# Kernel optimization log

Hardware: AMD Instinct MI355X
Metric: run time of the kernel (lower is better)

The kernel has to match this reference:

```python
import jax, jax.numpy as jnp
import numpy as np

B, T, D = 32, 1024, 512

def _xavier(key, shape):
    fan_in, fan_out = shape[1], shape[0]
    bound = float(np.sqrt(6.0 / (fan_in + fan_out)))
    return jax.random.uniform(key, shape, jnp.float32, -bound, bound)

def setup_inputs() -> dict:
    key = jax.random.key(0)
    ks = jax.random.split(key, 10)
    lin_bound = float(1.0 / np.sqrt(D))
    def lin(kw, kb):
        W = jax.random.uniform(kw, (D, D), jnp.float32, -lin_bound, lin_bound)
        b = jax.random.uniform(kb, (D,), jnp.float32, -lin_bound, lin_bound)
        return W, b
    Wk_w, Wk_b = lin(ks[0], ks[1])
    Wv_w, Wv_b = lin(ks[2], ks[3])
    Wq_w, Wq_b = lin(ks[4], ks[5])
    Wo_w, Wo_b = lin(ks[6], ks[7])
    w = _xavier(ks[8], (T, T))
    x = jax.random.normal(ks[9], (B, T, D), jnp.float32)
    return {"x": x, "Wk_w": Wk_w, "Wk_b": Wk_b, "Wv_w": Wv_w, "Wv_b": Wv_b,
            "Wq_w": Wq_w, "Wq_b": Wq_b, "w": w, "Wo_w": Wo_w, "Wo_b": Wo_b}

def reference(x, Wk_w, Wk_b, Wv_w, Wv_b, Wq_w, Wq_b, w, Wo_w, Wo_b):
    # K, V, Q: [B, T, D]  (torch Linear: x @ W.T + b)
    K = jnp.einsum('btd,ed->bte', x, Wk_w) + Wk_b
    V = jnp.einsum('btd,ed->bte', x, Wv_w) + Wv_b
    # exp_w: [T, T], row-wise max-stabilized position bias
    exp_w = jnp.exp(w - jnp.max(w, axis=-1, keepdims=True))
    # Faithful to original: max over dim=0 (batch dim) of K
    exp_K = jnp.exp(K - jnp.max(K, axis=0, keepdims=True))  # [B, T, D]
    num = jnp.einsum('ts,bsd->btd', exp_w, exp_K * V)
    den = jnp.einsum('ts,bsd->btd', exp_w, exp_K)
    Yt = num / den
    Q = jnp.einsum('btd,ed->bte', x, Wq_w) + Wq_b
    Yt = jax.nn.sigmoid(Q) * Yt
    out = jnp.einsum('btd,ed->bte', Yt, Wo_w) + Wo_b
    return out
```

## Files before the change

### kernel.cpp

```cpp
#include <hip/hip_runtime.h>
#include <stdint.h>

typedef unsigned short u16;
typedef __attribute__((ext_vector_type(4))) float f32x4;
typedef __attribute__((ext_vector_type(8))) __bf16 bf16x8;

__device__ __forceinline__ float b2f(u16 u) {
  union { unsigned int i; float f; } v; v.i = ((unsigned int)u) << 16; return v.f;
}
__device__ __forceinline__ u16 f2b(float f) {
  union { float f; unsigned int i; } v; v.f = f;
  unsigned int x = v.i;
  return (u16)((x + 0x7fffu + ((x >> 16) & 1u)) >> 16);
}

__device__ __forceinline__ void async_ld16(const u16* g, u16* l) {
  __builtin_amdgcn_global_load_lds((const __attribute__((address_space(1))) void*)g,
                                   (__attribute__((address_space(3))) void*)l, 16, 0, 0);
}

__global__ void detect_kernel(const u16* __restrict__ x, int* __restrict__ flag)
{
  const int tid = threadIdx.x;
  int found = 0;
  for (int i = tid; i < 32768; i += 256) {
    u16 u = x[i];
    if ((u & 0x7F80u) == 0x7F80u) found = 1;
  }
  unsigned long long m = __ballot(found != 0);
  __shared__ int sf[4];
  if ((tid & 63) == 0) sf[tid >> 6] = (m != 0ULL) ? 1 : 0;
  __syncthreads();
  if (tid == 0) flag[0] = (sf[0] | sf[1] | sf[2] | sf[3]);
}

__global__ __launch_bounds__(256)
void conv_kernel(const void* __restrict__ in, u16* __restrict__ out, long n,
                 const int* __restrict__ flag)
{
  const long i = ((long)blockIdx.x * 256 + threadIdx.x) * 8;
  if (i >= n) return;
  if (flag[0]) {
    const float* p = (const float*)in + i;
    u16 o[8];
#pragma unroll
    for (int j = 0; j < 8; j++) o[j] = f2b(p[j]);
    *(uint4*)(out + i) = *(const uint4*)o;
  } else {
    *(uint4*)(out + i) = *(const uint4*)((const u16*)in + i);
  }
}

__global__ __launch_bounds__(256)
void conv4_kernel(const void* __restrict__ i0, const void* __restrict__ i1,
                  const void* __restrict__ i2, const void* __restrict__ i3,
                  u16* __restrict__ o0, u16* __restrict__ o1,
                  u16* __restrict__ o2, u16* __restrict__ o3,
                  const int* __restrict__ flag)
{
  const int sel = blockIdx.x >> 7;
  const int blk = blockIdx.x & 127;
  const void* in = (sel == 0) ? i0 : (sel == 1) ? i1 : (sel == 2) ? i2 : i3;
  u16* out = (sel == 0) ? o0 : (sel == 1) ? o1 : (sel == 2) ? o2 : o3;
  const long i = ((long)blk * 256 + threadIdx.x) * 8;
  if (flag[0]) {
    const float* p = (const float*)in + i;
    u16 o[8];
#pragma unroll
    for (int j = 0; j < 8; j++) o[j] = f2b(p[j]);
    *(uint4*)(out + i) = *(const uint4*)o;
  } else {
    *(uint4*)(out + i) = *(const uint4*)((const u16*)in + i);
  }
}

#define BM 128
#define BN 128
#define BK 32

template<int EPI>
__global__ __launch_bounds__(256)
void gemm_bt(const u16* __restrict__ A, const u16* __restrict__ B,
             const void* __restrict__ bias, void* __restrict__ Cv,
             const int* __restrict__ flag,
             int M, int N, int K, long strideC)
{
  __shared__ __align__(16) u16 sA[2][BM * BK];
  __shared__ __align__(16) u16 sB[2][BN * BK];

  const int tid  = threadIdx.x;
  const int lane = tid & 63;
  const int wv   = tid >> 6;
  const int fl = flag[0];
  u16* Cb16 = (u16*)Cv;

  int bx = blockIdx.x, by = blockIdx.y;
  {
    const int nx = gridDim.x, ny = gridDim.y;
    if ((nx & 7) == 0) {
      const int d   = bx + nx * by;
      const int xcd = d & 7;
      const int s   = d >> 3;
      const int q   = s / ny;
      bx = xcd * (nx >> 3) + q;
      by = s - q * ny;
    }
  }
  const int m0 = bx * BM;
  const int n0 = by * BN;

  const int ldRow = wv * 32;
  const int lr = lane >> 2;
  const int lc = lane & 3;
  const int scol = (lc ^ ((lr >> 1) & 3)) * 8;
  const u16* gA = A + (long)(m0 + ldRow + lr) * K + scol;
  const u16* gB = B + (long)(n0 + ldRow + lr) * K + scol;
  const int off0 = (ldRow + lr) * BK + lc * 8;
  const int off1 = (ldRow + 16 + lr) * BK + lc * 8;

  f32x4 acc[4][4];
#pragma unroll
  for (int i = 0; i < 4; i++)
#pragma unroll
    for (int j = 0; j < 4; j++) acc[i][j] = (f32x4)0.0f;

  const int waveM = (wv >> 1) * 64;
  const int waveN = (wv & 1) * 64;
  const int quad  = lane >> 4;
  const int ll    = lane & 15;
  const int rs    = (quad ^ ((ll >> 1) & 3)) * 8;

  async_ld16(gA,          sA[0] + off0);
  async_ld16(gA + 16 * K, sA[0] + off1);
  async_ld16(gB,          sB[0] + off0);
  async_ld16(gB + 16 * K, sB[0] + off1);
  gA += BK; gB += BK;

  const int NT = K / BK;
  for (int t = 0; t < NT; ++t) {
    __syncthreads();
    const int cur = t & 1;
    if (t + 1 < NT) {
      u16* dA = sA[cur ^ 1];
      u16* dB = sB[cur ^ 1];
      async_ld16(gA,          dA + off0);
      async_ld16(gA + 16 * K, dA + off1);
      async_ld16(gB,          dB + off0);
      async_ld16(gB + 16 * K, dB + off1);
      gA += BK; gB += BK;
    }
    const u16* rA = sA[cur];
    const u16* rB = sB[cur];
    bf16x8 aF[4], bF[4];
#pragma unroll
    for (int i = 0; i < 4; i++) {
      aF[i] = *(const bf16x8*)(rA + (waveM + i * 16 + ll) * BK + rs);
      bF[i] = *(const bf16x8*)(rB + (waveN + i * 16 + ll) * BK + rs);
    }
#pragma unroll
    for (int i = 0; i < 4; i++)
#pragma unroll
      for (int j = 0; j < 4; j++)
        acc[i][j] = __builtin_amdgcn_mfma_f32_16x16x32_bf16(aF[i], bF[j], acc[i][j], 0, 0, 0);
  }

#pragma unroll
  for (int i = 0; i < 4; i++) {
    const int rowb = m0 + waveM + i * 16 + quad * 4;
#pragma unroll
    for (int j = 0; j < 4; j++) {
      const int col = n0 + waveN + j * 16 + ll;
      const float bv = fl ? ((const float*)bias)[col] : b2f(((const u16*)bias)[col]);
#pragma unroll
      for (int r = 0; r < 4; r++) {
        const long idx = (long)(rowb + r) * N + col;
        const float v = acc[i][j][r] + bv;
        if (EPI == 0) {
          Cb16[idx] = f2b(v);
        } else {
          const long g = strideC + idx;
          if (fl) ((float*)Cv)[g] = v;
          else    ((u16*)Cv)[g]   = f2b(v);
        }
      }
    }
  }
}

__global__ __launch_bounds__(256)
void gemm_proj3(const u16* __restrict__ A, const u16* __restrict__ Bw,
                const void* __restrict__ kb, const void* __restrict__ vb,
                const void* __restrict__ qb,
                u16* __restrict__ Kp, u16* __restrict__ Vp, u16* __restrict__ Qp,
                const int* __restrict__ flag, int M)
{
  const int KD = 512;
  __shared__ __align__(16) u16 sA[2][BM * BK];
  __shared__ __align__(16) u16 sB[2][BN * BK];

  const int tid  = threadIdx.x;
  const int lane = tid & 63;
  const int wv   = tid >> 6;
  const int fl = flag[0];

  int bx = blockIdx.x, by = blockIdx.y;
  {
    const int nx = gridDim.x, ny = gridDim.y;
    if ((nx & 7) == 0) {
      const int d   = bx + nx * by;
      const int xcd = d & 7;
      const int s   = d >> 3;
      const int q   = s / ny;
      bx = xcd * (nx >> 3) + q;
      by = s - q * ny;
    }
  }
  const int m0 = bx * BM;
  const int n0 = by * BN;

  const int ldRow = wv * 32;
  const int lr = lane >> 2;
  const int lc = lane & 3;
  const int scol = (lc ^ ((lr >> 1) & 3)) * 8;
  const u16* gA = A  + (long)(m0 + ldRow + lr) * KD + scol;
  const u16* gB = Bw + (long)(n0 + ldRow + lr) * KD + scol;
  const int off0 = (ldRow + lr) * BK + lc * 8;
  const int off1 = (ldRow + 16 + lr) * BK + lc * 8;

  f32x4 acc[4][4];
#pragma unroll
  for (int i = 0; i < 4; i++)
#pragma unroll
    for (int j = 0; j < 4; j++) acc[i][j] = (f32x4)0.0f;

  const int waveM = (wv >> 1) * 64;
  const int waveN = (wv & 1) * 64;
  const int quad  = lane >> 4;
  const int ll    = lane & 15;
  const int rs    = (quad ^ ((ll >> 1) & 3)) * 8;

  async_ld16(gA,           sA[0] + off0);
  async_ld16(gA + 16 * KD, sA[0] + off1);
  async_ld16(gB,           sB[0] + off0);
  async_ld16(gB + 16 * KD, sB[0] + off1);
  gA += BK; gB += BK;

  const int NT = KD / BK;
  for (int t = 0; t < NT; ++t) {
    __syncthreads();
    const int cur = t & 1;
    if (t + 1 < NT) {
      u16* dA = sA[cur ^ 1];
      u16* dB = sB[cur ^ 1];
      async_ld16(gA,           dA + off0);
      async_ld16(gA + 16 * KD, dA + off1);
      async_ld16(gB,           dB + off0);
      async_ld16(gB + 16 * KD, dB + off1);
      gA += BK; gB += BK;
    }
    const u16* rA = sA[cur];
    const u16* rB = sB[cur];
    bf16x8 aF[4], bF[4];
#pragma unroll
    for (int i = 0; i < 4; i++) {
      aF[i] = *(const bf16x8*)(rA + (waveM + i * 16 + ll) * BK + rs);
      bF[i] = *(const bf16x8*)(rB + (waveN + i * 16 + ll) * BK + rs);
    }
#pragma unroll
    for (int i = 0; i < 4; i++)
#pragma unroll
      for (int j = 0; j < 4; j++)
        acc[i][j] = __builtin_amdgcn_mfma_f32_16x16x32_bf16(aF[i], bF[j], acc[i][j], 0, 0, 0);
  }

#pragma unroll
  for (int i = 0; i < 4; i++) {
    const int rowb = m0 + waveM + i * 16 + quad * 4;
#pragma unroll
    for (int j = 0; j < 4; j++) {
      const int col = n0 + waveN + j * 16 + ll;
      const int sel = col >> 9;
      const int cs  = col & 511;
      const void* bp = (sel == 0) ? kb : (sel == 1) ? vb : qb;
      u16* dst = (sel == 0) ? Kp : (sel == 1) ? Vp : Qp;
      const float bv = fl ? ((const float*)bp)[cs] : b2f(((const u16*)bp)[cs]);
#pragma unroll
      for (int r = 0; r < 4; r++)
        dst[(long)(rowb + r) * 512 + cs] = f2b(acc[i][j][r] + bv);
    }
  }
}

__global__ __launch_bounds__(512, 2)
void gemm_aft(const u16* __restrict__ ew, const u16* __restrict__ Pt,
              const u16* __restrict__ PVt, const u16* __restrict__ Q,
              u16* __restrict__ Yt)
{
  const int T = 1024, D = 512;
  __shared__ __align__(16) u16 sA[2 * 2 * 256 * 32];
  __shared__ __align__(16) u16 sB[2 * 2 * 128 * 32];
  __shared__ __align__(16) u16 sC[2 * 2 * 128 * 32];

  const int tid  = threadIdx.x;
  const int lane = tid & 63;
  const int wv   = tid >> 6;

  int xt = blockIdx.x, yt = blockIdx.y, zt = blockIdx.z;
  {
    const int nz = gridDim.z;
    if ((nz & 1) == 0) {
      const int d   = xt + (yt << 2) + (zt << 4);
      const int xcd = d & 7;
      const int s   = d >> 3;
      xt = s & 3;
      const int p = xcd * (nz >> 1) + (s >> 2);
      yt = p & 3;
      zt = p >> 2;
    }
  }
  const int b = zt;
  const u16* Ptb  = Pt  + (long)b * D * T;
  const u16* PVtb = PVt + (long)b * D * T;
  const u16* Qb   = Q   + (long)b * T * D;
  u16*       Ytb  = Yt  + (long)b * T * D;
  const int m0 = xt * 256;
  const int n0 = yt * 128;

  const int sr = tid >> 2, ss = tid & 3;
  const int sslot = (ss ^ ((sr >> 1) & 3)) * 8;
  const u16* gA0 = ew   + (long)(m0 + sr)       * T + sslot;
  const u16* gA1 = ew   + (long)(m0 + 128 + sr) * T + sslot;
  const u16* gB  = Ptb  + (long)(n0 + sr)       * T + sslot;
  const u16* gC  = PVtb + (long)(n0 + sr)       * T + sslot;
  const int soff = sr * 32 + ss * 8;

  f32x4 accN[8][2], accD[8][2];
#pragma unroll
  for (int i = 0; i < 8; i++)
#pragma unroll
    for (int j = 0; j < 2; j++) { accN[i][j] = (f32x4)0.0f; accD[i][j] = (f32x4)0.0f; }

  const int quad  = lane >> 4;
  const int ll    = lane & 15;
  const int rs    = (quad ^ ((ll >> 1) & 3)) * 8;
  const int waveM = (wv >> 2) * 128;
  const int waveN = (wv & 3) * 32;

  async_ld16(gA0,      sA + soff);
  async_ld16(gA1,      sA + 4096 + soff);
  async_ld16(gB,       sB + soff);
  async_ld16(gC,       sC + soff);
  async_ld16(gA0 + 32, sA + 8192 + soff);
  async_ld16(gA1 + 32, sA + 8192 + 4096 + soff);
  async_ld16(gB  + 32, sB + 4096 + soff);
  async_ld16(gC  + 32, sC + 4096 + soff);
  asm volatile("s_waitcnt vmcnt(4)" ::: "memory");
  __builtin_amdgcn_s_barrier();

  const int NT = T / 64;
  for (int t = 0; t < NT; ++t) {
    const int cur = t & 1;
    const u16* bA = sA + cur * 16384;
    const u16* bB = sB + cur * 8192;
    const u16* bC = sC + cur * 8192;
    u16* nA = sA + (cur ^ 1) * 16384;
    u16* nB = sB + (cur ^ 1) * 8192;
    u16* nC = sC + (cur ^ 1) * 8192;
    const int ko = (t + 1) * 64;
    const bool st = (t + 1 < NT);

    bf16x8 aF[4], bF[2], cF[2];

#pragma unroll
    for (int i = 0; i < 4; i++)
      aF[i] = *(const bf16x8*)(bA + (waveM + i * 16 + ll) * 32 + rs);
#pragma unroll
    for (int j = 0; j < 2; j++) {
      bF[j] = *(const bf16x8*)(bB + (waveN + j * 16 + ll) * 32 + rs);
      cF[j] = *(const bf16x8*)(bC + (waveN + j * 16 + ll) * 32 + rs);
    }
    if (st) {
      async_ld16(gA0 + ko, nA + soff);
      async_ld16(gA1 + ko, nA + 4096 + soff);
    }
    __builtin_amdgcn_s_barrier();
    asm volatile("s_waitcnt lgkmcnt(0)" ::: "memory");
    __builtin_amdgcn_sched_barrier(0);
    __builtin_amdgcn_s_setprio(1);
#pragma unroll
    for (int i = 0; i < 4; i++)
#pragma unroll
      for (int j = 0; j < 2; j++) {
        accD[i][j] = __builtin_amdgcn_mfma_f32_16x16x32_bf16(aF[i], bF[j], accD[i][j], 0, 0, 0);
        accN[i][j] = __builtin_amdgcn_mfma_f32_16x16x32_bf16(aF[i], cF[j], accN[i][j], 0, 0, 0);
      }
    __builtin_amdgcn_s_setprio(0);
    __builtin_amdgcn_s_barrier();

#pragma unroll
    for (int i = 0; i < 4; i++)
      aF[i] = *(const bf16x8*)(bA + (waveM + (4 + i) * 16 + ll) * 32 + rs);
    if (st) {
      async_ld16(gB + ko, nB + soff);
      async_ld16(gC + ko, nC + soff);
    }
    __builtin_amdgcn_s_barrier();
    asm volatile("s_waitcnt lgkmcnt(0)" ::: "memory");
    __builtin_amdgcn_sched_barrier(0);
    __builtin_amdgcn_s_setprio(1);
#pragma unroll
    for (int i = 0; i < 4; i++)
#pragma unroll
      for (int j = 0; j < 2; j++) {
        accD[4 + i][j] = __builtin_amdgcn_mfma_f32_16x16x32_bf16(aF[i], bF[j], accD[4 + i][j], 0, 0, 0);
        accN[4 + i][j] = __builtin_amdgcn_mfma_f32_16x16x32_bf16(aF[i], cF[j], accN[4 + i][j], 0, 0, 0);
      }
    __builtin_amdgcn_s_setprio(0);
    if (st) asm volatile("s_waitcnt vmcnt(4)" ::: "memory");
    else    asm volatile("s_waitcnt vmcnt(0)" ::: "memory");
    __builtin_amdgcn_s_barrier();

    const u16* bA1 = bA + 8192;
    const u16* bB1 = bB + 4096;
    const u16* bC1 = bC + 4096;
#pragma unroll
    for (int i = 0; i < 4; i++)
      aF[i] = *(const bf16x8*)(bA1 + (waveM + i * 16 + ll) * 32 + rs);
#pragma unroll
    for (int j = 0; j < 2; j++) {
      bF[j] = *(const bf16x8*)(bB1 + (waveN + j * 16 + ll) * 32 + rs);
      cF[j] = *(const bf16x8*)(bC1 + (waveN + j * 16 + ll) * 32 + rs);
    }
    if (st) {
      async_ld16(gA0 + ko + 32, nA + 8192 + soff);
      async_ld16(gA1 + ko + 32, nA + 8192 + 4096 + soff);
    }
    __builtin_amdgcn_s_barrier();
    asm volatile("s_waitcnt lgkmcnt(0)" ::: "memory");
    __builtin_amdgcn_sched_barrier(0);
    __builtin_amdgcn_s_setprio(1);
#pragma unroll
    for (int i = 0; i < 4; i++)
#pragma unroll
      for (int j = 0; j < 2; j++) {
        accD[i][j] = __builtin_amdgcn_mfma_f32_16x16x32_bf16(aF[i], bF[j], accD[i][j], 0, 0, 0);
        accN[i][j] = __builtin_amdgcn_mfma_f32_16x16x32_bf16(aF[i], cF[j], accN[i][j], 0, 0, 0);
      }
    __builtin_amdgcn_s_setprio(0);
    __builtin_amdgcn_s_barrier();

#pragma unroll
    for (int i = 0; i < 4; i++)
      aF[i] = *(const bf16x8*)(bA1 + (waveM + (4 + i) * 16 + ll) * 32 + rs);
    if (st) {
      async_ld16(gB + ko + 32, nB + 4096 + soff);
      async_ld16(gC + ko + 32, nC + 4096 + soff);
    }
    __builtin_amdgcn_s_barrier();
    asm volatile("s_waitcnt lgkmcnt(0)" ::: "memory");
    __builtin_amdgcn_sched_barrier(0);
    __builtin_amdgcn_s_setprio(1);
#pragma unroll
    for (int i = 0; i < 4; i++)
#pragma unroll
      for (int j = 0; j < 2; j++) {
        accD[4 + i][j] = __builtin_amdgcn_mfma_f32_16x16x32_bf16(aF[i], bF[j], accD[4 + i][j], 0, 0, 0);
        accN[4 + i][j] = __builtin_amdgcn_mfma_f32_16x16x32_bf16(aF[i], cF[j], accN[4 + i][j], 0, 0, 0);
      }
    __builtin_amdgcn_s_setprio(0);
    if (st) asm volatile("s_waitcnt vmcnt(4)" ::: "memory");
    else    asm volatile("s_waitcnt vmcnt(0)" ::: "memory");
    __builtin_amdgcn_s_barrier();
  }

#pragma unroll
  for (int i = 0; i < 8; i++) {
    const int rowb = m0 + waveM + i * 16 + quad * 4;
#pragma unroll
    for (int j = 0; j < 2; j++) {
      const int col = n0 + waveN + j * 16 + ll;
#pragma unroll
      for (int r = 0; r < 4; r++) {
        const long idx = (long)(rowb + r) * D + col;
        const float q  = b2f(Qb[idx]);
        const float e  = __expf(-q);
        const float rc = __builtin_amdgcn_rcpf(accD[i][j][r] * (1.0f + e));
        Ytb[idx] = f2b(accN[i][j][r] * rc);
      }
    }
  }
}

__global__ __launch_bounds__(256)
void expw_kernel(const void* __restrict__ w, u16* __restrict__ ew,
                 const int* __restrict__ flag)
{
  const int fl = flag[0];
  const int t = blockIdx.x;
  const int tid = threadIdx.x;
  float v[4];
  float m = -1e30f;
#pragma unroll
  for (int i = 0; i < 4; i++) {
    const long idx = (long)t * 1024 + tid + i * 256;
    float val = fl ? ((const float*)w)[idx] : b2f(((const u16*)w)[idx]);
    v[i] = val; m = fmaxf(m, val);
  }
#pragma unroll
  for (int off = 32; off > 0; off >>= 1) m = fmaxf(m, __shfl_xor(m, off, 64));
  __shared__ float sm[4];
  if ((tid & 63) == 0) sm[tid >> 6] = m;
  __syncthreads();
  m = fmaxf(fmaxf(sm[0], sm[1]), fmaxf(sm[2], sm[3]));
  u16* orow = ew + (long)t * 1024;
#pragma unroll
  for (int i = 0; i < 4; i++) orow[tid + i * 256] = f2b(__expf(v[i] - m));
}

__global__ __launch_bounds__(256)
void kmax_kernel(const u16* __restrict__ K, u16* __restrict__ Km)
{
  const long TD = 1024L * 512;
  const long base = ((long)blockIdx.x * 256 + threadIdx.x) * 8;
  float m[8];
#pragma unroll
  for (int j = 0; j < 8; j++) m[j] = -1e30f;
  for (int b = 0; b < 32; b++) {
    uint4 u = *(const uint4*)(K + b * TD + base);
    const u16* p = (const u16*)&u;
#pragma unroll
    for (int j = 0; j < 8; j++) m[j] = fmaxf(m[j], b2f(p[j]));
  }
  u16 outv[8];
#pragma unroll
  for (int j = 0; j < 8; j++) outv[j] = f2b(m[j]);
  *(uint4*)(Km + base) = *(const uint4*)outv;
}

__global__ __launch_bounds__(256)
void pexp_kernel(const u16* __restrict__ K, const u16* __restrict__ V,
                 const u16* __restrict__ Km,
                 u16* __restrict__ Pt, u16* __restrict__ PVt)
{
  const int T = 1024, D = 512;
  const long TD = (long)T * D;
  const int s0 = blockIdx.x * 64;
  const int d0 = blockIdx.y * 64;
  const int b  = blockIdx.z;
  __shared__ u16 lp[64 * 66];
  __shared__ u16 lpv[64 * 66];
  const int tid  = threadIdx.x;
  const int srow = tid >> 3;
  const int c8   = (tid & 7) * 8;

#pragma unroll
  for (int h = 0; h < 2; h++) {
    const int s = srow + h * 32;
    const long gidx = (long)b * TD + (long)(s0 + s) * D + d0 + c8;
    uint4 ku = *(const uint4*)(K + gidx);
    uint4 vu = *(const uint4*)(V + gidx);
    uint4 mu = *(const uint4*)(Km + (long)(s0 + s) * D + d0 + c8);
    const u16* kp = (const u16*)&ku;
    const u16* vp = (const u16*)&vu;
    const u16* mp = (const u16*)&mu;
#pragma unroll
    for (int j = 0; j < 8; j++) {
      float p  = __expf(b2f(kp[j]) - b2f(mp[j]));
      float pv = p * b2f(vp[j]);
      lp[s * 66 + c8 + j]  = f2b(p);
      lpv[s * 66 + c8 + j] = f2b(pv);
    }
  }
  __syncthreads();

  const int lane = tid & 63;
  const int wv   = tid >> 6;
#pragma unroll
  for (int it = 0; it < 16; it++) {
    const int d = wv * 16 + it;
    const long oidx = (long)b * TD + (long)(d0 + d) * T + s0 + lane;
    Pt[oidx]  = lp[lane * 66 + d];
    PVt[oidx] = lpv[lane * 66 + d];
  }
}

extern "C" void kernel_launch(void* const* d_in, const int* in_sizes, int n_in,
                              void* d_out, int out_size, void* d_ws, size_t ws_size,
                              hipStream_t stream)
{
  const int B = 32, T = 1024, D = 512;
  const long TD = (long)T * D;
  const void* x    = d_in[0];
  const void* Wk_w = d_in[1];
  const void* Wk_b = d_in[2];
  const void* Wv_w = d_in[3];
  const void* Wv_b = d_in[4];
  const void* Wq_w = d_in[5];
  const void* Wq_b = d_in[6];
  const void* w    = d_in[7];
  const void* Wo_w = d_in[8];
  const void* Wo_b = d_in[9];

  char* ws = (char*)d_ws;
  const size_t MB = 1024 * 1024;
  u16* xb    = (u16*)(ws + 0);
  u16* Kbuf  = (u16*)(ws + 32 * MB);
  u16* ewb   = (u16*)(ws + 64 * MB);
  u16* kmb   = (u16*)(ws + 66 * MB);
  u16* Wpack = (u16*)(ws + 67 * MB);
  u16* Wvb   = Wpack + 512 * 512;
  u16* Wqb   = Wpack + 2 * 512 * 512;
  u16* Wob   = (u16*)(ws + 68 * MB + 512 * 1024);
  int* flag  = (int*)(ws + 69 * MB);
  u16* Ytb   = Kbuf;

  dim3 blk(256);

  detect_kernel<<<dim3(1), blk, 0, stream>>>((const u16*)x, flag);
  conv_kernel<<<dim3(8192), blk, 0, stream>>>(x, xb, (long)B * T * D, flag);
  conv4_kernel<<<dim3(512), blk, 0, stream>>>(Wk_w, Wv_w, Wq_w, Wo_w,
                                              Wpack, Wvb, Wqb, Wob, flag);
  expw_kernel<<<dim3(1024), blk, 0, stream>>>(w, ewb, flag);

  if (ws_size >= 200 * MB) {
    u16* Vb   = (u16*)(ws + 70 * MB);
    u16* Qb   = (u16*)(ws + 102 * MB);
    u16* Ptb  = (u16*)(ws + 134 * MB);
    u16* PVtb = (u16*)(ws + 166 * MB);

    gemm_proj3<<<dim3((B * T) / 128, 12), blk, 0, stream>>>(
        xb, Wpack, Wk_b, Wv_b, Wq_b, Kbuf, Vb, Qb, flag, B * T);

    kmax_kernel<<<dim3(256), blk, 0, stream>>>(Kbuf, kmb);
    pexp_kernel<<<dim3(16, 8, 32), blk, 0, stream>>>(Kbuf, Vb, kmb, Ptb, PVtb);

    gemm_aft<<<dim3(4, 4, 32), dim3(512), 0, stream>>>(ewb, Ptb, PVtb, Qb, Ytb);

    gemm_bt<3><<<dim3((B * T) / 128, D / 128), blk, 0, stream>>>(
        Ytb, Wob, Wo_b, d_out, flag, B * T, D, D, 0);
  } else {
    const int NB = 4, NC = B / NB;
    char* ck = ws + 70 * MB;
    const size_t cb = (size_t)NB * TD * sizeof(u16);
    u16* Vc   = (u16*)(ck);
    u16* Ptc  = (u16*)(ck + cb);
    u16* PVtc = (u16*)(ck + 2 * cb);
    u16* Qc   = (u16*)(ck + 3 * cb);
    u16* Ytc  = Vc;

    gemm_bt<0><<<dim3((B * T) / 128, D / 128), blk, 0, stream>>>(
        xb, Wpack, Wk_b, Kbuf, flag, B * T, D, D, 0);
    kmax_kernel<<<dim3(256), blk, 0, stream>>>(Kbuf, kmb);

    dim3 gP((NB * T) / 128, D / 128, 1);
    dim3 gA(4, 4, NB);
    for (int c = 0; c < NC; c++) {
      const long off = (long)c * NB * TD;
      gemm_bt<0><<<gP, blk, 0, stream>>>(xb + off, Wvb, Wv_b, Vc, flag, NB * T, D, D, 0);
      gemm_bt<0><<<gP, blk, 0, stream>>>(xb + off, Wqb, Wq_b, Qc, flag, NB * T, D, D, 0);
      pexp_kernel<<<dim3(16, 8, NB), blk, 0, stream>>>(Kbuf + off, Vc, kmb, Ptc, PVtc);
      gemm_aft<<<gA, dim3(512), 0, stream>>>(ewb, Ptc, PVtc, Qc, Ytc);
      gemm_bt<3><<<gP, blk, 0, stream>>>(Ytc, Wob, Wo_b, d_out, flag, NB * T, D, D, off);
    }
  }
}
```

Baseline: 378.2 us.

## Fuse x conversion into projection GEMM, merge prep kernels, add 256x256 output GEMM

The projection GEMM now reads x directly (fp32 or bf16) through registers and converts to bf16 before storing to LDS, so the separate full-size conversion pass over x is gone on the large-workspace path. The weight conversion and exp(w) kernels are merged into a single prep launch. The output projection moves to a new 256x256-tile, 512-thread GEMM with finer-grained async prefetch and priority hints. The trade-off is that the projection kernel's A operand now goes through synchronous register loads instead of async global-to-LDS copies.

```diff
diff --git a/kernel.cpp b/kernel.cpp
--- a/kernel.cpp
+++ b/kernel.cpp
@@ -52,25 +52,49 @@
 }
 
 __global__ __launch_bounds__(256)
-void conv4_kernel(const void* __restrict__ i0, const void* __restrict__ i1,
-                  const void* __restrict__ i2, const void* __restrict__ i3,
-                  u16* __restrict__ o0, u16* __restrict__ o1,
-                  u16* __restrict__ o2, u16* __restrict__ o3,
-                  const int* __restrict__ flag)
-{
-  const int sel = blockIdx.x >> 7;
-  const int blk = blockIdx.x & 127;
-  const void* in = (sel == 0) ? i0 : (sel == 1) ? i1 : (sel == 2) ? i2 : i3;
-  u16* out = (sel == 0) ? o0 : (sel == 1) ? o1 : (sel == 2) ? o2 : o3;
-  const long i = ((long)blk * 256 + threadIdx.x) * 8;
-  if (flag[0]) {
-    const float* p = (const float*)in + i;
-    u16 o[8];
-#pragma unroll
-    for (int j = 0; j < 8; j++) o[j] = f2b(p[j]);
-    *(uint4*)(out + i) = *(const uint4*)o;
+void prep_kernel(const void* __restrict__ i0, const void* __restrict__ i1,
+                 const void* __restrict__ i2, const void* __restrict__ i3,
+                 u16* __restrict__ o0, u16* __restrict__ o1,
+                 u16* __restrict__ o2, u16* __restrict__ o3,
+                 const void* __restrict__ w, u16* __restrict__ ew,
+                 const int* __restrict__ flag)
+{
+  const int fl = flag[0];
+  const int tid = threadIdx.x;
+  if (blockIdx.x < 512) {
+    const int sel = blockIdx.x >> 7;
+    const int blk = blockIdx.x & 127;
+    const void* in = (sel == 0) ? i0 : (sel == 1) ? i1 : (sel == 2) ? i2 : i3;
+    u16* out = (sel == 0) ? o0 : (sel == 1) ? o1 : (sel == 2) ? o2 : o3;
+    const long i = ((long)blk * 256 + tid) * 8;
+    if (fl) {
+      const float* p = (const float*)in + i;
+      u16 o[8];
+#pragma unroll
+      for (int j = 0; j < 8; j++) o[j] = f2b(p[j]);
+      *(uint4*)(out + i) = *(const uint4*)o;
+    } else {
+      *(uint4*)(out + i) = *(const uint4*)((const u16*)in + i);
+    }
   } else {
-    *(uint4*)(out + i) = *(const uint4*)((const u16*)in + i);
+    const int t = blockIdx.x - 512;
+    float v[4];
+    float m = -1e30f;
+#pragma unroll
+    for (int i = 0; i < 4; i++) {
+      const long idx = (long)t * 1024 + tid + i * 256;
+      float val = fl ? ((const float*)w)[idx] : b2f(((const u16*)w)[idx]);
+      v[i] = val; m = fmaxf(m, val);
+    }
+#pragma unroll
+    for (int off = 32; off > 0; off >>= 1) m = fmaxf(m, __shfl_xor(m, off, 64));
+    __shared__ float sm[4];
+    if ((tid & 63) == 0) sm[tid >> 6] = m;
+    __syncthreads();
+    m = fmaxf(fmaxf(sm[0], sm[1]), fmaxf(sm[2], sm[3]));
+    u16* orow = ew + (long)t * 1024;
+#pragma unroll
+    for (int i = 0; i < 4; i++) orow[tid + i * 256] = f2b(__expf(v[i] - m));
   }
 }
 
@@ -188,7 +212,7 @@
 }
 
 __global__ __launch_bounds__(256)
-void gemm_proj3(const u16* __restrict__ A, const u16* __restrict__ Bw,
+void gemm_proj3(const void* __restrict__ Xv, const u16* __restrict__ Bw,
                 const void* __restrict__ kb, const void* __restrict__ vb,
                 const void* __restrict__ qb,
                 u16* __restrict__ Kp, u16* __restrict__ Vp, u16* __restrict__ Qp,
@@ -206,14 +230,12 @@
   int bx = blockIdx.x, by = blockIdx.y;
   {
     const int nx = gridDim.x, ny = gridDim.y;
-    if ((nx & 7) == 0) {
-      const int d   = bx + nx * by;
-      const int xcd = d & 7;
-      const int s   = d >> 3;
-      const int q   = s / ny;
-      bx = xcd * (nx >> 3) + q;
-      by = s - q * ny;
-    }
+    const int d   = bx + nx * by;
+    const int xcd = d & 7;
+    const int s   = d >> 3;
+    const int q   = s / ny;
+    bx = xcd * (nx >> 3) + q;
+    by = s - q * ny;
   }
   const int m0 = bx * BM;
   const int n0 = by * BN;
@@ -222,7 +244,10 @@
   const int lr = lane >> 2;
   const int lc = lane & 3;
   const int scol = (lc ^ ((lr >> 1) & 3)) * 8;
-  const u16* gA = A  + (long)(m0 + ldRow + lr) * KD + scol;
+  const long arow0 = (long)(m0 + ldRow + lr) * KD + scol;
+  const long arow1 = (long)(m0 + ldRow + 16 + lr) * KD + scol;
+  const float* gAf = (const float*)Xv;
+  const u16*   gAh = (const u16*)Xv;
   const u16* gB = Bw + (long)(n0 + ldRow + lr) * KD + scol;
   const int off0 = (ldRow + lr) * BK + lc * 8;
   const int off1 = (ldRow + 16 + lr) * BK + lc * 8;
@@ -239,25 +264,57 @@
   const int ll    = lane & 15;
   const int rs    = (quad ^ ((ll >> 1) & 3)) * 8;
 
-  async_ld16(gA,           sA[0] + off0);
-  async_ld16(gA + 16 * KD, sA[0] + off1);
+  f32x4 af0, af1, af2, af3;
+  uint4 ah0, ah1;
+  if (fl) {
+    af0 = *(const f32x4*)(gAf + arow0);
+    af1 = *(const f32x4*)(gAf + arow0 + 4);
+    af2 = *(const f32x4*)(gAf + arow1);
+    af3 = *(const f32x4*)(gAf + arow1 + 4);
+  } else {
+    ah0 = *(const uint4*)(gAh + arow0);
+    ah1 = *(const uint4*)(gAh + arow1);
+  }
   async_ld16(gB,           sB[0] + off0);
   async_ld16(gB + 16 * KD, sB[0] + off1);
-  gA += BK; gB += BK;
+  gB += BK;
 
   const int NT = KD / BK;
   for (int t = 0; t < NT; ++t) {
+    const int cur = t & 1;
+    uint4 w0, w1;
+    if (fl) {
+      u16 o0[8], o1[8];
+#pragma unroll
+      for (int j = 0; j < 4; j++) {
+        o0[j] = f2b(af0[j]); o0[4 + j] = f2b(af1[j]);
+        o1[j] = f2b(af2[j]); o1[4 + j] = f2b(af3[j]);
+      }
+      w0 = *(const uint4*)o0; w1 = *(const uint4*)o1;
+    } else {
+      w0 = ah0; w1 = ah1;
+    }
+    *(uint4*)(sA[cur] + off0) = w0;
+    *(uint4*)(sA[cur] + off1) = w1;
     __syncthreads();
-    const int cur = t & 1;
+
     if (t + 1 < NT) {
-      u16* dA = sA[cur ^ 1];
+      const int ko = (t + 1) * BK;
+      if (fl) {
+        af0 = *(const f32x4*)(gAf + arow0 + ko);
+        af1 = *(const f32x4*)(gAf + arow0 + ko + 4);
+        af2 = *(const f32x4*)(gAf + arow1 + ko);
+        af3 = *(const f32x4*)(gAf + arow1 + ko + 4);
+      } else {
+        ah0 = *(const uint4*)(gAh + arow0 + ko);
+        ah1 = *(const uint4*)(gAh + arow1 + ko);
+      }
       u16* dB = sB[cur ^ 1];
-      async_ld16(gA,           dA + off0);
-      async_ld16(gA + 16 * KD, dA + off1);
       async_ld16(gB,           dB + off0);
       async_ld16(gB + 16 * KD, dB + off1);
-      gA += BK; gB += BK;
-    }
+      gB += BK;
+    }
+
     const u16* rA = sA[cur];
     const u16* rB = sB[cur];
     bf16x8 aF[4], bF[4];
@@ -287,6 +344,181 @@
 #pragma unroll
       for (int r = 0; r < 4; r++)
         dst[(long)(rowb + r) * 512 + cs] = f2b(acc[i][j][r] + bv);
+    }
+  }
+}
+
+__global__ __launch_bounds__(512, 2)
+void gemm_out8(const u16* __restrict__ A, const u16* __restrict__ Bw,
+               const void* __restrict__ bias, void* __restrict__ Cv,
+               const int* __restrict__ flag, int M, int N, int K)
+{
+  __shared__ __align__(16) u16 sA[2 * 2 * 256 * 32];
+  __shared__ __align__(16) u16 sB[2 * 2 * 256 * 32];
+
+  const int tid  = threadIdx.x;
+  const int lane = tid & 63;
+  const int wv   = tid >> 6;
+  const int fl = flag[0];
+
+  int bx = blockIdx.x, by = blockIdx.y;
+  {
+    const int nx = gridDim.x, ny = gridDim.y;
+    const int d   = bx + nx * by;
+    const int xcd = d & 7;
+    const int s   = d >> 3;
+    const int q   = s / ny;
+    bx = xcd * (nx >> 3) + q;
+    by = s - q * ny;
+  }
+  const int m0 = bx * 256;
+  const int n0 = by * 256;
+
+  const int sr = tid >> 2, ss = tid & 3;
+  const int sslot = (ss ^ ((sr >> 1) & 3)) * 8;
+  const u16* gA0 = A  + (long)(m0 + sr)       * K + sslot;
+  const u16* gA1 = A  + (long)(m0 + 128 + sr) * K + sslot;
+  const u16* gB0 = Bw + (long)(n0 + sr)       * K + sslot;
+  const u16* gB1 = Bw + (long)(n0 + 128 + sr) * K + sslot;
+  const int soff = sr * 32 + ss * 8;
+
+  f32x4 acc[8][4];
+#pragma unroll
+  for (int i = 0; i < 8; i++)
+#pragma unroll
+    for (int j = 0; j < 4; j++) acc[i][j] = (f32x4)0.0f;
+
+  const int quad  = lane >> 4;
+  const int ll    = lane & 15;
+  const int rs    = (quad ^ ((ll >> 1) & 3)) * 8;
+  const int waveM = (wv >> 2) * 128;
+  const int waveN = (wv & 3) * 64;
+
+  async_ld16(gA0,      sA + soff);
+  async_ld16(gA1,      sA + 4096 + soff);
+  async_ld16(gB0,      sB + soff);
+  async_ld16(gB1,      sB + 4096 + soff);
+  async_ld16(gA0 + 32, sA + 8192 + soff);
+  async_ld16(gA1 + 32, sA + 8192 + 4096 + soff);
+  async_ld16(gB0 + 32, sB + 8192 + soff);
+  async_ld16(gB1 + 32, sB + 8192 + 4096 + soff);
+  asm volatile("s_waitcnt vmcnt(4)" ::: "memory");
+  __builtin_amdgcn_s_barrier();
+
+  const int NT = K / 64;
+  for (int t = 0; t < NT; ++t) {
+    const int cur = t & 1;
+    const u16* bA = sA + cur * 16384;
+    const u16* bB = sB + cur * 16384;
+    u16* nA = sA + (cur ^ 1) * 16384;
+    u16* nB = sB + (cur ^ 1) * 16384;
+    const int ko = (t + 1) * 64;
+    const bool st = (t + 1 < NT);
+    bf16x8 aF[4], bF[4];
+
+#pragma unroll
+    for (int i = 0; i < 4; i++)
+      aF[i] = *(const bf16x8*)(bA + (waveM + i * 16 + ll) * 32 + rs);
+#pragma unroll
+    for (int j = 0; j < 4; j++)
+      bF[j] = *(const bf16x8*)(bB + (waveN + j * 16 + ll) * 32 + rs);
+    if (st) {
+      async_ld16(gA0 + ko, nA + soff);
+      async_ld16(gA1 + ko, nA + 4096 + soff);
+    }
+    __builtin_amdgcn_s_barrier();
+    asm volatile("s_waitcnt lgkmcnt(0)" ::: "memory");
+    __builtin_amdgcn_sched_barrier(0);
+    __builtin_amdgcn_s_setprio(1);
+#pragma unroll
+    for (int i = 0; i < 4; i++)
+#pragma unroll
+      for (int j = 0; j < 4; j++)
+        acc[i][j] = __builtin_amdgcn_mfma_f32_16x16x32_bf16(aF[i], bF[j], acc[i][j], 0, 0, 0);
+    __builtin_amdgcn_s_setprio(0);
+    __builtin_amdgcn_s_barrier();
+
+#pragma unroll
+    for (int i = 0; i < 4; i++)
+      aF[i] = *(const bf16x8*)(bA + (waveM + (4 + i) * 16 + ll) * 32 + rs);
+    if (st) {
+      async_ld16(gB0 + ko, nB + soff);
+      async_ld16(gB1 + ko, nB + 4096 + soff);
+    }
+    __builtin_amdgcn_s_barrier();
+    asm volatile("s_waitcnt lgkmcnt(0)" ::: "memory");
+    __builtin_amdgcn_sched_barrier(0);
+    __builtin_amdgcn_s_setprio(1);
+#pragma unroll
+    for (int i = 0; i < 4; i++)
+#pragma unroll
+      for (int j = 0; j < 4; j++)
+        acc[4 + i][j] = __builtin_amdgcn_mfma_f32_16x16x32_bf16(aF[i], bF[j], acc[4 + i][j], 0, 0, 0);
+    __builtin_amdgcn_s_setprio(0);
+    if (st) asm volatile("s_waitcnt vmcnt(4)" ::: "memory");
+    else    asm volatile("s_waitcnt vmcnt(0)" ::: "memory");
+    __builtin_amdgcn_s_barrier();
+
+    const u16* bA1 = bA + 8192;
+    const u16* bB1 = bB + 8192;
+#pragma unroll
+    for (int i = 0; i < 4; i++)
+      aF[i] = *(const bf16x8*)(bA1 + (waveM + i * 16 + ll) * 32 + rs);
+#pragma unroll
+    for (int j = 0; j < 4; j++)
+      bF[j] = *(const bf16x8*)(bB1 + (waveN + j * 16 + ll) * 32 + rs);
+    if (st) {
+      async_ld16(gA0 + ko + 32, nA + 8192 + soff);
+      async_ld16(gA1 + ko + 32, nA + 8192 + 4096 + soff);
+    }
+    __builtin_amdgcn_s_barrier();
+    asm volatile("s_waitcnt lgkmcnt(0)" ::: "memory");
+    __builtin_amdgcn_sched_barrier(0);
+    __builtin_amdgcn_s_setprio(1);
+#pragma unroll
+    for (int i = 0; i < 4; i++)
+#pragma unroll
+      for (int j = 0; j < 4; j++)
+        acc[i][j] = __builtin_amdgcn_mfma_f32_16x16x32_bf16(aF[i], bF[j], acc[i][j], 0, 0, 0);
+    __builtin_amdgcn_s_setprio(0);
+    __builtin_amdgcn_s_barrier();
+
+#pragma unroll
+    for (int i = 0; i < 4; i++)
+      aF[i] = *(const bf16x8*)(bA1 + (waveM + (4 + i) * 16 + ll) * 32 + rs);
+    if (st) {
+      async_ld16(gB0 + ko + 32, nB + 8192 + soff);
+      async_ld16(gB1 + ko + 32, nB + 8192 + 4096 + soff);
+    }
+    __builtin_amdgcn_s_barrier();
+    asm volatile("s_waitcnt lgkmcnt(0)" ::: "memory");
+    __builtin_amdgcn_sched_barrier(0);
+    __builtin_amdgcn_s_setprio(1);
+#pragma unroll
+    for (int i = 0; i < 4; i++)
+#pragma unroll
+      for (int j = 0; j < 4; j++)
+        acc[4 + i][j] = __builtin_amdgcn_mfma_f32_16x16x32_bf16(aF[i], bF[j], acc[4 + i][j], 0, 0, 0);
+    __builtin_amdgcn_s_setprio(0);
+    if (st) asm volatile("s_waitcnt vmcnt(4)" ::: "memory");
+    else    asm volatile("s_waitcnt vmcnt(0)" ::: "memory");
+    __builtin_amdgcn_s_barrier();
+  }
+
+#pragma unroll
+  for (int i = 0; i < 8; i++) {
+    const int rowb = m0 + waveM + i * 16 + quad * 4;
+#pragma unroll
+    for (int j = 0; j < 4; j++) {
+      const int col = n0 + waveN + j * 16 + ll;
+      const float bv = fl ? ((const float*)bias)[col] : b2f(((const u16*)bias)[col]);
+#pragma unroll
+      for (int r = 0; r < 4; r++) {
+        const long idx = (long)(rowb + r) * N + col;
+        const float v = acc[i][j][r] + bv;
+        if (fl) ((float*)Cv)[idx] = v;
+        else    ((u16*)Cv)[idx]   = f2b(v);
+      }
     }
   }
 }
@@ -489,32 +721,6 @@
       }
     }
   }
-}
-
-__global__ __launch_bounds__(256)
-void expw_kernel(const void* __restrict__ w, u16* __restrict__ ew,
-                 const int* __restrict__ flag)
-{
-  const int fl = flag[0];
-  const int t = blockIdx.x;
-  const int tid = threadIdx.x;
-  float v[4];
-  float m = -1e30f;
-#pragma unroll
-  for (int i = 0; i < 4; i++) {
-    const long idx = (long)t * 1024 + tid + i * 256;
-    float val = fl ? ((const float*)w)[idx] : b2f(((const u16*)w)[idx]);
-    v[i] = val; m = fmaxf(m, val);
-  }
-#pragma unroll
-  for (int off = 32; off > 0; off >>= 1) m = fmaxf(m, __shfl_xor(m, off, 64));
-  __shared__ float sm[4];
-  if ((tid & 63) == 0) sm[tid >> 6] = m;
-  __syncthreads();
-  m = fmaxf(fmaxf(sm[0], sm[1]), fmaxf(sm[2], sm[3]));
-  u16* orow = ew + (long)t * 1024;
-#pragma unroll
-  for (int i = 0; i < 4; i++) orow[tid + i * 256] = f2b(__expf(v[i] - m));
 }
 
 __global__ __launch_bounds__(256)
@@ -617,10 +823,9 @@
   dim3 blk(256);
 
   detect_kernel<<<dim3(1), blk, 0, stream>>>((const u16*)x, flag);
-  conv_kernel<<<dim3(8192), blk, 0, stream>>>(x, xb, (long)B * T * D, flag);
-  conv4_kernel<<<dim3(512), blk, 0, stream>>>(Wk_w, Wv_w, Wq_w, Wo_w,
-                                              Wpack, Wvb, Wqb, Wob, flag);
-  expw_kernel<<<dim3(1024), blk, 0, stream>>>(w, ewb, flag);
+  prep_kernel<<<dim3(1536), blk, 0, stream>>>(Wk_w, Wv_w, Wq_w, Wo_w,
+                                              Wpack, Wvb, Wqb, Wob,
+                                              w, ewb, flag);
 
   if (ws_size >= 200 * MB) {
     u16* Vb   = (u16*)(ws + 70 * MB);
@@ -629,15 +834,15 @@
     u16* PVtb = (u16*)(ws + 166 * MB);
 
     gemm_proj3<<<dim3((B * T) / 128, 12), blk, 0, stream>>>(
-        xb, Wpack, Wk_b, Wv_b, Wq_b, Kbuf, Vb, Qb, flag, B * T);
+        x, Wpack, Wk_b, Wv_b, Wq_b, Kbuf, Vb, Qb, flag, B * T);
 
     kmax_kernel<<<dim3(256), blk, 0, stream>>>(Kbuf, kmb);
     pexp_kernel<<<dim3(16, 8, 32), blk, 0, stream>>>(Kbuf, Vb, kmb, Ptb, PVtb);
 
     gemm_aft<<<dim3(4, 4, 32), dim3(512), 0, stream>>>(ewb, Ptb, PVtb, Qb, Ytb);
 
-    gemm_bt<3><<<dim3((B * T) / 128, D / 128), blk, 0, stream>>>(
-        Ytb, Wob, Wo_b, d_out, flag, B * T, D, D, 0);
+    gemm_out8<<<dim3((B * T) / 256, 2), dim3(512), 0, stream>>>(
+        Ytb, Wob, Wo_b, d_out, flag, B * T, D, D);
   } else {
     const int NB = 4, NC = B / NB;
     char* ck = ws + 70 * MB;
@@ -648,6 +853,7 @@
     u16* Qc   = (u16*)(ck + 3 * cb);
     u16* Ytc  = Vc;
 
+    conv_kernel<<<dim3(8192), blk, 0, stream>>>(x, xb, (long)B * T * D, flag);
     gemm_bt<0><<<dim3((B * T) / 128, D / 128), blk, 0, stream>>>(
         xb, Wpack, Wk_b, Kbuf, flag, B * T, D, D, 0);
     kmax_kernel<<<dim3(256), blk, 0, stream>>>(Kbuf, kmb);
```

Measured after the change: 395.0 us. 1.04x slower.
